# Kernel tuning notes

Hardware: AMD Instinct MI355X
Metric: run time of the kernel (lower is better)

## Reference

```python
import jax, jax.numpy as jnp
import numpy as np

N_HEAD = 16
D_MODEL = 1024
D_K = D_MODEL // N_HEAD  # 64
LN_EPS = 1e-5


def setup_inputs() -> dict:
    key = jax.random.key(0)
    ks = jax.random.split(key, 12)
    B, L, D = 4, 2048, D_MODEL
    std_qkv = float(np.sqrt(2.0 / (D + D_K)))
    q = jax.random.normal(ks[0], (B, L, D), jnp.float32)
    k = jax.random.normal(ks[1], (B, L, D), jnp.float32)
    v = jax.random.normal(ks[2], (B, L, D), jnp.float32)
    Wq = jax.random.normal(ks[3], (D, D), jnp.float32) * std_qkv
    Wk = jax.random.normal(ks[4], (D, D), jnp.float32) * std_qkv
    Wv = jax.random.normal(ks[5], (D, D), jnp.float32) * std_qkv
    bq = jnp.zeros((D,), jnp.float32)
    bk = jnp.zeros((D,), jnp.float32)
    bv = jnp.zeros((D,), jnp.float32)
    # xavier normal for fc: std = sqrt(2/(fan_in+fan_out))
    Wo = jax.random.normal(ks[6], (D, D), jnp.float32) * float(np.sqrt(2.0 / (D + D)))
    bo = jnp.zeros((D,), jnp.float32)
    gamma = jnp.ones((D,), jnp.float32)
    beta = jnp.zeros((D,), jnp.float32)
    return {"q": q, "k": k, "v": v, "Wq": Wq, "bq": bq, "Wk": Wk, "bk": bk,
            "Wv": Wv, "bv": bv, "Wo": Wo, "bo": bo, "gamma": gamma, "beta": beta}


def _layer_norm(x, gamma, beta):
    mu = jnp.mean(x, axis=-1, keepdims=True)
    var = jnp.mean(jnp.square(x - mu), axis=-1, keepdims=True)
    return (x - mu) * jax.lax.rsqrt(var + LN_EPS) * gamma + beta


def reference(q, k, v, Wq, bq, Wk, bk, Wv, bv, Wo, bo, gamma, beta):
    B, Lq, D = q.shape
    Lk = k.shape[1]
    h, dk = N_HEAD, D_K
    residual = q
    # projections (torch Linear: x @ W.T + b), split heads -> (h, b, l, dk)
    qh = (q @ Wq.T + bq).reshape(B, Lq, h, dk).transpose(2, 0, 1, 3)
    kh = (k @ Wk.T + bk).reshape(B, Lk, h, dk).transpose(2, 0, 1, 3)
    vh = (v @ Wv.T + bv).reshape(B, Lk, h, dk).transpose(2, 0, 1, 3)
    temp = jnp.asarray(np.power(dk, 0.5), qh.dtype)
    scores = jnp.einsum('hbqd,hbkd->hbqk', qh, kh) / temp
    attn = jax.nn.softmax(scores, axis=-1)  # softmax over key dim (dim=2 of bmm view)
    out = jnp.einsum('hbqk,hbkd->hbqd', attn, vh)
    # (h,b,lq,dk) -> (b,lq,h*dk)
    out = out.transpose(1, 2, 0, 3).reshape(B, Lq, D)
    out = out @ Wo.T + bo  # dropout p=0.0 -> identity
    out = _layer_norm(out + residual, gamma, beta)
    attn_flat = attn.reshape(h * B, Lq, Lk)  # matches torch (n_head*sz_b, lq, lk)
    return out, attn_flat
```

## Files before the change

### kernel.cpp

```cpp
#include <hip/hip_runtime.h>
#include <stdint.h>

typedef short bf16x8 __attribute__((ext_vector_type(8)));
typedef float f32x4 __attribute__((ext_vector_type(4)));
typedef unsigned short us4 __attribute__((ext_vector_type(4)));
typedef unsigned short us8 __attribute__((ext_vector_type(8)));
typedef unsigned uint2v __attribute__((ext_vector_type(2)));

#define SCL 0.18033688011112042f

__device__ __forceinline__ unsigned short f2bf(float f) {
  union { float f; unsigned u; } v; v.f = f;
  unsigned r = v.u + 0x7fffu + ((v.u >> 16) & 1u);
  return (unsigned short)(r >> 16);
}

__device__ __forceinline__ unsigned cvtpk(float lo, float hi) {
  unsigned r;
  asm("v_cvt_pk_bf16_f32 %0, %1, %2" : "=v"(r) : "v"(lo), "v"(hi));
  return r;
}

__device__ __forceinline__ float bf2f(unsigned short h) {
  union { unsigned u; float f; } v; v.u = ((unsigned)h) << 16; return v.f;
}

#define GL2LDS(g, l) __builtin_amdgcn_global_load_lds( \
    (const __attribute__((address_space(1))) void*)(g), \
    (__attribute__((address_space(3))) void*)(l), 16, 0, 0)

__global__ __launch_bounds__(256) void convert_all(
    const float* __restrict__ q, const float* __restrict__ k, const float* __restrict__ v,
    const float* __restrict__ wq, const float* __restrict__ wk, const float* __restrict__ wv,
    const float* __restrict__ wo,
    unsigned short* __restrict__ qb, unsigned short* __restrict__ kb, unsigned short* __restrict__ vb,
    unsigned short* __restrict__ wqb, unsigned short* __restrict__ wkb, unsigned short* __restrict__ wvb,
    unsigned short* __restrict__ wob)
{
  const long NB = 8388608, NW = 1048576;
  long i = ((long)blockIdx.x * 256 + threadIdx.x) * 4;
  if (i >= 3*NB + 4*NW) return;
  const float* src; unsigned short* dst; long off;
  if (i < NB)              { src = q;  dst = qb;  off = i; }
  else if (i < 2*NB)       { src = k;  dst = kb;  off = i - NB; }
  else if (i < 3*NB)       { src = v;  dst = vb;  off = i - 2*NB; }
  else if (i < 3*NB+NW)    { src = wq; dst = wqb; off = i - 3*NB; }
  else if (i < 3*NB+2*NW)  { src = wk; dst = wkb; off = i - 3*NB - NW; }
  else if (i < 3*NB+3*NW)  { src = wv; dst = wvb; off = i - 3*NB - 2*NW; }
  else                     { src = wo; dst = wob; off = i - 3*NB - 3*NW; }
  float4 x = *(const float4*)(src + off);
  us4 o; o.x = f2bf(x.x); o.y = f2bf(x.y); o.z = f2bf(x.z); o.w = f2bf(x.w);
  *(us4*)(dst + off) = o;
}

__global__ __launch_bounds__(256, 2) void qkv_gemm(
    const unsigned short* __restrict__ qb, const unsigned short* __restrict__ kb,
    const unsigned short* __restrict__ vb,
    const unsigned short* __restrict__ wqb, const unsigned short* __restrict__ wkb,
    const unsigned short* __restrict__ wvb,
    const float* __restrict__ bq, const float* __restrict__ bk, const float* __restrict__ bv,
    unsigned short* __restrict__ qh, unsigned short* __restrict__ kh,
    unsigned short* __restrict__ vt)
{
  const int z = blockIdx.z;
  const unsigned short* X = (z == 0) ? qb : (z == 1) ? kb : vb;
  const unsigned short* W = (z == 0) ? wqb : (z == 1) ? wkb : wvb;
  const float* bias = (z == 0) ? bq : (z == 1) ? bk : bv;
  unsigned short* dqh = (z == 0) ? qh : kh;
  const float sc = (z == 0) ? SCL : 1.0f;

  const int flat = blockIdx.x + (blockIdx.y << 6);
  const int xcd = flat & 7, ii = flat >> 3;
  const int m0 = (xcd * 8 + (ii & 7)) * 128;
  const int n0 = (ii >> 3) * 128;

  const int tid = threadIdx.x, lane = tid & 63, w = tid >> 6;
  const int wr = w >> 1, wc = w & 1;
  const int lg = lane >> 4, ll = lane & 15;

  __shared__ __align__(16) unsigned short As[2 * 128 * 32];
  __shared__ __align__(16) unsigned short Bs[2 * 128 * 32];

  f32x4 acc[4][4] = {};

  const char* gA = (const char*)X + ((size_t)(m0 + w*32 + (lane >> 2)) * 1024) * 2 + (lane & 3) * 16;
  const char* gB = (const char*)W + ((size_t)(n0 + w*32 + (lane >> 2)) * 1024) * 2 + (lane & 3) * 16;

#define STAGE_G(buf) do { \
    char* lA_ = (char*)As + (buf)*8192 + w*2048; \
    char* lB_ = (char*)Bs + (buf)*8192 + w*2048; \
    GL2LDS(gA, lA_); GL2LDS(gA + 32768, lA_ + 1024); \
    GL2LDS(gB, lB_); GL2LDS(gB + 32768, lB_ + 1024); \
    gA += 64; gB += 64; } while (0)

  STAGE_G(0);
  __syncthreads();

  for (int k0 = 0; k0 < 1024; k0 += 32) {
    const int cur = (k0 >> 5) & 1;
    if (k0 < 992) STAGE_G(cur ^ 1);
    const unsigned short* Ac = As + cur * 4096;
    const unsigned short* Bc = Bs + cur * 4096;
    bf16x8 xa[4], wb[4];
    const int kc = lg * 8;
#pragma unroll
    for (int f = 0; f < 4; ++f) xa[f] = *(const bf16x8*)&Ac[(wr*64 + f*16 + ll)*32 + kc];
#pragma unroll
    for (int f = 0; f < 4; ++f) wb[f] = *(const bf16x8*)&Bc[(wc*64 + f*16 + ll)*32 + kc];
    if (z < 2) {
#pragma unroll
      for (int fn = 0; fn < 4; ++fn)
#pragma unroll
        for (int fm = 0; fm < 4; ++fm)
          acc[fn][fm] = __builtin_amdgcn_mfma_f32_16x16x32_bf16(wb[fn], xa[fm], acc[fn][fm], 0, 0, 0);
    } else {
#pragma unroll
      for (int fm = 0; fm < 4; ++fm)
#pragma unroll
        for (int fn = 0; fn < 4; ++fn)
          acc[fm][fn] = __builtin_amdgcn_mfma_f32_16x16x32_bf16(xa[fm], wb[fn], acc[fm][fn], 0, 0, 0);
    }
    __syncthreads();
  }

  if (z < 2) {
#pragma unroll
    for (int fn = 0; fn < 4; ++fn) {
      const int n_g = n0 + wc*64 + fn*16 + lg*4;
      const float4 b4 = *(const float4*)&bias[n_g];
      const int h = n_g >> 6, dkk = n_g & 63;
#pragma unroll
      for (int fm = 0; fm < 4; ++fm) {
        const int m_g = m0 + wr*64 + fm*16 + ll;
        const int b_ = m_g >> 11, l_ = m_g & 2047;
        us4 pk;
        pk.x = f2bf((acc[fn][fm][0] + b4.x) * sc);
        pk.y = f2bf((acc[fn][fm][1] + b4.y) * sc);
        pk.z = f2bf((acc[fn][fm][2] + b4.z) * sc);
        pk.w = f2bf((acc[fn][fm][3] + b4.w) * sc);
        *(us4*)&dqh[((size_t)(h*4 + b_) * 2048 + l_) * 64 + dkk] = pk;
      }
    }
  } else {
#pragma unroll
    for (int fn = 0; fn < 4; ++fn) {
      const int n_g = n0 + wc*64 + fn*16 + ll;
      const float bias_n = bias[n_g];
      const int h = n_g >> 6, dkk = n_g & 63;
#pragma unroll
      for (int fm = 0; fm < 4; ++fm) {
        const int mrow = m0 + wr*64 + fm*16 + lg*4;
        const int b_ = mrow >> 11, l_ = mrow & 2047;
        us4 pk;
        pk.x = f2bf(acc[fm][fn][0] + bias_n);
        pk.y = f2bf(acc[fm][fn][1] + bias_n);
        pk.z = f2bf(acc[fm][fn][2] + bias_n);
        pk.w = f2bf(acc[fm][fn][3] + bias_n);
        *(us4*)&vt[((size_t)(h*4 + b_) * 64 + dkk) * 2048 + l_] = pk;
      }
    }
  }
}

__global__ __launch_bounds__(256, 2) void attn_kernel(
    const unsigned short* __restrict__ qh, const unsigned short* __restrict__ kh,
    const unsigned short* __restrict__ vt, float* __restrict__ probs,
    unsigned short* __restrict__ attn_o)
{
  const int bid = blockIdx.x;
  const int xcd = bid & 7;
  const int idx = bid >> 3;
  const int hb  = xcd * 8 + (idx & 7);
  const int qp  = idx >> 3;
  const int qt_a = qp * 2, qt_b = qp * 2 + 1;

  const int tid = threadIdx.x, lane = tid & 63, w = tid >> 6;
  const int wr = w >> 1, wc = w & 1;
  const int lg = lane >> 4, ll = lane & 15;

  __shared__ __align__(16) char smem[38400];
  unsigned short* Pb = (unsigned short*)smem;
  float* rs   = (float*)(smem + 36864);
  float* invl = (float*)(smem + 37888);
  float* Ored = (float*)smem;

  const size_t slab = (size_t)hb << 17;

  bf16x8 qfa[4][2], qfb[4][2];
#pragma unroll
  for (int fq = 0; fq < 4; ++fq)
#pragma unroll
    for (int dh = 0; dh < 2; ++dh) {
      qfa[fq][dh] = *(const bf16x8*)&qh[slab + (size_t)(qt_a*128 + wr*64 + fq*16 + ll)*64 + dh*32 + lg*8];
      qfb[fq][dh] = *(const bf16x8*)&qh[slab + (size_t)(qt_b*128 + wr*64 + fq*16 + ll)*64 + dh*32 + lg*8];
    }

  const unsigned short* Kf = kh + slab + (size_t)(wc*32 + ll)*64 + lg*8;
  const unsigned short* Vf = vt + slab + (size_t)ll*2048 + wc*32 + lg*8;

  const int prow = tid >> 4, pcol = (tid & 15) * 4;

  float rsum[4] = {0.f, 0.f, 0.f, 0.f};
  for (int kt = 0; kt < 32; ++kt) {
    bf16x8 ka[2][2];
#pragma unroll
    for (int fk = 0; fk < 2; ++fk)
#pragma unroll
      for (int dh = 0; dh < 2; ++dh)
        ka[fk][dh] = *(const bf16x8*)(Kf + kt*4096 + fk*1024 + dh*32);
    f32x4 s[2][4] = {};
    __builtin_amdgcn_s_setprio(1);
#pragma unroll
    for (int dh = 0; dh < 2; ++dh)
#pragma unroll
      for (int fk = 0; fk < 2; ++fk)
#pragma unroll
        for (int fq = 0; fq < 4; ++fq)
          s[fk][fq] = __builtin_amdgcn_mfma_f32_16x16x32_bf16(ka[fk][dh], qfa[fq][dh], s[fk][fq], 0, 0, 0);
    __builtin_amdgcn_s_setprio(0);
#pragma unroll
    for (int fk = 0; fk < 2; ++fk)
#pragma unroll
      for (int fq = 0; fq < 4; ++fq)
#pragma unroll
        for (int r = 0; r < 4; ++r)
          rsum[fq] += exp2f(s[fk][fq][r]);
  }

#pragma unroll
  for (int fq = 0; fq < 4; ++fq) {
    float t = rsum[fq];
    t += __shfl_xor(t, 16);
    t += __shfl_xor(t, 32);
    rsum[fq] = t;
  }
  if (lg == 0) {
#pragma unroll
    for (int fq = 0; fq < 4; ++fq)
      rs[wc*128 + wr*64 + fq*16 + ll] = rsum[fq];
  }
  __syncthreads();
  if (tid < 128) invl[tid] = 1.0f / (rs[tid] + rs[128 + tid]);
  __syncthreads();
  float inv_ra[4];
#pragma unroll
  for (int fq = 0; fq < 4; ++fq) inv_ra[fq] = invl[wr*64 + fq*16 + ll];
  __syncthreads();

  f32x4 o[4][4] = {};
  float rsb[4] = {0.f, 0.f, 0.f, 0.f};
  float* pb2a = probs + ((size_t)hb << 22) + (size_t)(qt_a*128) * 2048;

  for (int kt = 0; kt < 32; ++kt) {
    unsigned short* Pc = Pb + (kt & 1) * 9216;
    bf16x8 vb[4];
#pragma unroll
    for (int f = 0; f < 4; ++f)
      vb[f] = *(const bf16x8*)(Vf + f*32768 + kt*64);
    bf16x8 ka[2][2];
#pragma unroll
    for (int fk = 0; fk < 2; ++fk)
#pragma unroll
      for (int dh = 0; dh < 2; ++dh)
        ka[fk][dh] = *(const bf16x8*)(Kf + kt*4096 + fk*1024 + dh*32);

    {
      f32x4 sb[2][4] = {};
      __builtin_amdgcn_s_setprio(1);
#pragma unroll
      for (int dh = 0; dh < 2; ++dh)
#pragma unroll
        for (int fk = 0; fk < 2; ++fk)
#pragma unroll
          for (int fq = 0; fq < 4; ++fq)
            sb[fk][fq] = __builtin_amdgcn_mfma_f32_16x16x32_bf16(ka[fk][dh], qfb[fq][dh], sb[fk][fq], 0, 0, 0);
      __builtin_amdgcn_s_setprio(0);
#pragma unroll
      for (int fk = 0; fk < 2; ++fk)
#pragma unroll
        for (int fq = 0; fq < 4; ++fq)
#pragma unroll
          for (int r = 0; r < 4; ++r)
            rsb[fq] += exp2f(sb[fk][fq][r]);
    }

    f32x4 s[2][4] = {};
    __builtin_amdgcn_s_setprio(1);
#pragma unroll
    for (int dh = 0; dh < 2; ++dh)
#pragma unroll
      for (int fk = 0; fk < 2; ++fk)
#pragma unroll
        for (int fq = 0; fq < 4; ++fq)
          s[fk][fq] = __builtin_amdgcn_mfma_f32_16x16x32_bf16(ka[fk][dh], qfa[fq][dh], s[fk][fq], 0, 0, 0);
    __builtin_amdgcn_s_setprio(0);
#pragma unroll
    for (int fk = 0; fk < 2; ++fk)
#pragma unroll
      for (int fq = 0; fq < 4; ++fq) {
        float p0 = exp2f(s[fk][fq][0]) * inv_ra[fq];
        float p1 = exp2f(s[fk][fq][1]) * inv_ra[fq];
        float p2 = exp2f(s[fk][fq][2]) * inv_ra[fq];
        float p3 = exp2f(s[fk][fq][3]) * inv_ra[fq];
        uint2v u; u.x = cvtpk(p0, p1); u.y = cvtpk(p2, p3);
        *(uint2v*)&Pc[(wr*64 + fq*16 + ll)*72 + wc*32 + fk*16 + lg*4] = u;
      }
    __syncthreads();

    bf16x8 pa[4];
#pragma unroll
    for (int fm = 0; fm < 4; ++fm)
      pa[fm] = *(const bf16x8*)&Pc[(wr*64 + fm*16 + ll)*72 + wc*32 + lg*8];
    __builtin_amdgcn_s_setprio(1);
#pragma unroll
    for (int fm = 0; fm < 4; ++fm)
#pragma unroll
      for (int fd = 0; fd < 4; ++fd)
        o[fm][fd] = __builtin_amdgcn_mfma_f32_16x16x32_bf16(pa[fm], vb[fd], o[fm][fd], 0, 0, 0);
    __builtin_amdgcn_s_setprio(0);

    float* pdst = pb2a + kt*64;
#pragma unroll
    for (int j = 0; j < 8; ++j) {
      const int row = j*16 + prow;
      us4 pv = *(const us4*)&Pc[row*72 + pcol];
      f32x4 pf; pf[0] = bf2f(pv.x); pf[1] = bf2f(pv.y); pf[2] = bf2f(pv.z); pf[3] = bf2f(pv.w);
      __builtin_nontemporal_store(pf, (f32x4*)(pdst + (size_t)row*2048 + pcol));
    }
  }

  __syncthreads();
#pragma unroll
  for (int fq = 0; fq < 4; ++fq) {
    float t = rsb[fq];
    t += __shfl_xor(t, 16);
    t += __shfl_xor(t, 32);
    rsb[fq] = t;
  }
  if (lg == 0) {
#pragma unroll
    for (int fq = 0; fq < 4; ++fq)
      rs[wc*128 + wr*64 + fq*16 + ll] = rsb[fq];
  }
  if (wc == 1) {
#pragma unroll
    for (int fm = 0; fm < 4; ++fm)
#pragma unroll
      for (int fd = 0; fd < 4; ++fd)
#pragma unroll
        for (int r = 0; r < 4; ++r)
          Ored[wr*4096 + (fm*16 + lg*4 + r)*64 + fd*16 + ll] = o[fm][fd][r];
  }
  __syncthreads();
  if (tid < 128) invl[tid] = 1.0f / (rs[tid] + rs[128 + tid]);
  if (wc == 0) {
    const int b_ = hb & 3, h = hb >> 2;
#pragma unroll
    for (int fm = 0; fm < 4; ++fm)
#pragma unroll
      for (int fd = 0; fd < 4; ++fd)
#pragma unroll
        for (int r = 0; r < 4; ++r) {
          const int qrow = fm*16 + lg*4 + r;
          const int d = fd*16 + ll;
          float val = o[fm][fd][r] + Ored[wr*4096 + qrow*64 + d];
          const int mg = b_*2048 + qt_a*128 + wr*64 + qrow;
          attn_o[(size_t)mg*1024 + h*64 + d] = f2bf(val);
        }
  }
  __syncthreads();
  float inv_rb[4];
#pragma unroll
  for (int fq = 0; fq < 4; ++fq) inv_rb[fq] = invl[wr*64 + fq*16 + ll];
  __syncthreads();

#pragma unroll
  for (int fm = 0; fm < 4; ++fm)
#pragma unroll
    for (int fd = 0; fd < 4; ++fd)
      o[fm][fd] = f32x4{0.f, 0.f, 0.f, 0.f};
  float* pb2b = probs + ((size_t)hb << 22) + (size_t)(qt_b*128) * 2048;

  for (int kt = 0; kt < 32; ++kt) {
    unsigned short* Pc = Pb + (kt & 1) * 9216;
    bf16x8 vb[4];
#pragma unroll
    for (int f = 0; f < 4; ++f)
      vb[f] = *(const bf16x8*)(Vf + f*32768 + kt*64);
    bf16x8 ka[2][2];
#pragma unroll
    for (int fk = 0; fk < 2; ++fk)
#pragma unroll
      for (int dh = 0; dh < 2; ++dh)
        ka[fk][dh] = *(const bf16x8*)(Kf + kt*4096 + fk*1024 + dh*32);

    f32x4 s[2][4] = {};
    __builtin_amdgcn_s_setprio(1);
#pragma unroll
    for (int dh = 0; dh < 2; ++dh)
#pragma unroll
      for (int fk = 0; fk < 2; ++fk)
#pragma unroll
        for (int fq = 0; fq < 4; ++fq)
          s[fk][fq] = __builtin_amdgcn_mfma_f32_16x16x32_bf16(ka[fk][dh], qfb[fq][dh], s[fk][fq], 0, 0, 0);
    __builtin_amdgcn_s_setprio(0);

#pragma unroll
    for (int fk = 0; fk < 2; ++fk)
#pragma unroll
      for (int fq = 0; fq < 4; ++fq) {
        float p0 = exp2f(s[fk][fq][0]) * inv_rb[fq];
        float p1 = exp2f(s[fk][fq][1]) * inv_rb[fq];
        float p2 = exp2f(s[fk][fq][2]) * inv_rb[fq];
        float p3 = exp2f(s[fk][fq][3]) * inv_rb[fq];
        uint2v u; u.x = cvtpk(p0, p1); u.y = cvtpk(p2, p3);
        *(uint2v*)&Pc[(wr*64 + fq*16 + ll)*72 + wc*32 + fk*16 + lg*4] = u;
      }
    __syncthreads();

    bf16x8 pa[4];
#pragma unroll
    for (int fm = 0; fm < 4; ++fm)
      pa[fm] = *(const bf16x8*)&Pc[(wr*64 + fm*16 + ll)*72 + wc*32 + lg*8];
    __builtin_amdgcn_s_setprio(1);
#pragma unroll
    for (int fm = 0; fm < 4; ++fm)
#pragma unroll
      for (int fd = 0; fd < 4; ++fd)
        o[fm][fd] = __builtin_amdgcn_mfma_f32_16x16x32_bf16(pa[fm], vb[fd], o[fm][fd], 0, 0, 0);
    __builtin_amdgcn_s_setprio(0);

    float* pdst = pb2b + kt*64;
#pragma unroll
    for (int j = 0; j < 8; ++j) {
      const int row = j*16 + prow;
      us4 pv = *(const us4*)&Pc[row*72 + pcol];
      f32x4 pf; pf[0] = bf2f(pv.x); pf[1] = bf2f(pv.y); pf[2] = bf2f(pv.z); pf[3] = bf2f(pv.w);
      __builtin_nontemporal_store(pf, (f32x4*)(pdst + (size_t)row*2048 + pcol));
    }
  }

  __syncthreads();
  if (wc == 1) {
#pragma unroll
    for (int fm = 0; fm < 4; ++fm)
#pragma unroll
      for (int fd = 0; fd < 4; ++fd)
#pragma unroll
        for (int r = 0; r < 4; ++r)
          Ored[wr*4096 + (fm*16 + lg*4 + r)*64 + fd*16 + ll] = o[fm][fd][r];
  }
  __syncthreads();
  if (wc == 0) {
    const int b_ = hb & 3, h = hb >> 2;
#pragma unroll
    for (int fm = 0; fm < 4; ++fm)
#pragma unroll
      for (int fd = 0; fd < 4; ++fd)
#pragma unroll
        for (int r = 0; r < 4; ++r) {
          const int qrow = fm*16 + lg*4 + r;
          const int d = fd*16 + ll;
          float val = o[fm][fd][r] + Ored[wr*4096 + qrow*64 + d];
          const int mg = b_*2048 + qt_b*128 + wr*64 + qrow;
          attn_o[(size_t)mg*1024 + h*64 + d] = f2bf(val);
        }
  }
}

__global__ __launch_bounds__(256, 2) void outproj_gemm(
    const unsigned short* __restrict__ Ain, const unsigned short* __restrict__ Wob,
    const float* __restrict__ bo, const float* __restrict__ qres, float* __restrict__ preLN)
{
  const int flat = blockIdx.x + (blockIdx.y << 6);
  const int xcd = flat & 7, ii = flat >> 3;
  const int m0 = (xcd * 8 + (ii & 7)) * 128;
  const int n0 = (ii >> 3) * 128;

  const int tid = threadIdx.x, lane = tid & 63, w = tid >> 6;
  const int wr = w >> 1, wc = w & 1;
  const int lg = lane >> 4, ll = lane & 15;

  __shared__ __align__(16) unsigned short As[2 * 128 * 32];
  __shared__ __align__(16) unsigned short Bs[2 * 128 * 32];

  f32x4 acc[4][4] = {};

  const char* gA = (const char*)Ain + ((size_t)(m0 + w*32 + (lane >> 2)) * 1024) * 2 + (lane & 3) * 16;
  const char* gB = (const char*)Wob + ((size_t)(n0 + w*32 + (lane >> 2)) * 1024) * 2 + (lane & 3) * 16;

  STAGE_G(0);
  __syncthreads();

  for (int k0 = 0; k0 < 1024; k0 += 32) {
    const int cur = (k0 >> 5) & 1;
    if (k0 < 992) STAGE_G(cur ^ 1);
    const unsigned short* Ac = As + cur * 4096;
    const unsigned short* Bc = Bs + cur * 4096;
    bf16x8 xa[4], wb[4];
    const int kc = lg * 8;
#pragma unroll
    for (int f = 0; f < 4; ++f) xa[f] = *(const bf16x8*)&Ac[(wr*64 + f*16 + ll)*32 + kc];
#pragma unroll
    for (int f = 0; f < 4; ++f) wb[f] = *(const bf16x8*)&Bc[(wc*64 + f*16 + ll)*32 + kc];
#pragma unroll
    for (int fn = 0; fn < 4; ++fn)
#pragma unroll
      for (int fm = 0; fm < 4; ++fm)
        acc[fn][fm] = __builtin_amdgcn_mfma_f32_16x16x32_bf16(wb[fn], xa[fm], acc[fn][fm], 0, 0, 0);
    __syncthreads();
  }

#pragma unroll
  for (int fn = 0; fn < 4; ++fn) {
    const int n_g = n0 + wc*64 + fn*16 + lg*4;
    const float4 b4 = *(const float4*)&bo[n_g];
#pragma unroll
    for (int fm = 0; fm < 4; ++fm) {
      const int m_g = m0 + wr*64 + fm*16 + ll;
      const size_t idxp = (size_t)m_g * 1024 + n_g;
      const float4 r4 = *(const float4*)&qres[idxp];
      f32x4 y;
      y[0] = acc[fn][fm][0] + b4.x + r4.x;
      y[1] = acc[fn][fm][1] + b4.y + r4.y;
      y[2] = acc[fn][fm][2] + b4.z + r4.z;
      y[3] = acc[fn][fm][3] + b4.w + r4.w;
      *(f32x4*)&preLN[idxp] = y;
    }
  }
}

__global__ __launch_bounds__(256) void ln_kernel(
    const float* __restrict__ x, const float* __restrict__ gamma,
    const float* __restrict__ beta, float* __restrict__ out)
{
  const int row = blockIdx.x, tid = threadIdx.x;
  const float4 xv = ((const float4*)(x + (size_t)row * 1024))[tid];
  float s = xv.x + xv.y + xv.z + xv.w;
  float ss = xv.x*xv.x + xv.y*xv.y + xv.z*xv.z + xv.w*xv.w;
#pragma unroll
  for (int m = 1; m < 64; m <<= 1) { s += __shfl_xor(s, m); ss += __shfl_xor(ss, m); }
  __shared__ float red[8];
  if ((tid & 63) == 0) { red[(tid >> 6)*2] = s; red[(tid >> 6)*2 + 1] = ss; }
  __syncthreads();
  s  = red[0] + red[2] + red[4] + red[6];
  ss = red[1] + red[3] + red[5] + red[7];
  const float mu = s * (1.0f/1024.0f);
  const float var = ss * (1.0f/1024.0f) - mu*mu;
  const float rstd = rsqrtf(var + 1e-5f);
  const float4 g  = ((const float4*)gamma)[tid];
  const float4 be = ((const float4*)beta)[tid];
  float4 y;
  y.x = (xv.x - mu)*rstd*g.x + be.x;
  y.y = (xv.y - mu)*rstd*g.y + be.y;
  y.z = (xv.z - mu)*rstd*g.z + be.z;
  y.w = (xv.w - mu)*rstd*g.w + be.w;
  ((float4*)(out + (size_t)row * 1024))[tid] = y;
}

extern "C" void kernel_launch(void* const* d_in, const int* in_sizes, int n_in,
                              void* d_out, int out_size, void* d_ws, size_t ws_size,
                              hipStream_t stream) {
  const float* q     = (const float*)d_in[0];
  const float* k     = (const float*)d_in[1];
  const float* v     = (const float*)d_in[2];
  const float* Wq    = (const float*)d_in[3];
  const float* bq    = (const float*)d_in[4];
  const float* Wk    = (const float*)d_in[5];
  const float* bk    = (const float*)d_in[6];
  const float* Wv    = (const float*)d_in[7];
  const float* bv    = (const float*)d_in[8];
  const float* Wo    = (const float*)d_in[9];
  const float* bo    = (const float*)d_in[10];
  const float* gamma = (const float*)d_in[11];
  const float* beta  = (const float*)d_in[12];

  float* out   = (float*)d_out;
  float* probs = out + 8388608;

  char* ws = (char*)d_ws;
  unsigned short* qb  = (unsigned short*)(ws);
  unsigned short* kb  = (unsigned short*)(ws + 16777216);
  unsigned short* vb  = (unsigned short*)(ws + 33554432);
  unsigned short* wqb = (unsigned short*)(ws + 50331648);
  unsigned short* wkb = (unsigned short*)(ws + 52428800);
  unsigned short* wvb = (unsigned short*)(ws + 54525952);
  unsigned short* wob = (unsigned short*)(ws + 56623104);
  unsigned short* qh  = (unsigned short*)(ws + 58720256);
  unsigned short* kh  = (unsigned short*)(ws + 75497472);
  unsigned short* vt  = (unsigned short*)(ws + 92274688);
  float* preLN = (float*)(ws);
  unsigned short* attn_o = vb;

  convert_all<<<28672, 256, 0, stream>>>(q, k, v, Wq, Wk, Wv, Wo,
                                         qb, kb, vb, wqb, wkb, wvb, wob);

  dim3 g1(64, 8, 3);
  qkv_gemm<<<g1, 256, 0, stream>>>(qb, kb, vb, wqb, wkb, wvb, bq, bk, bv, qh, kh, vt);

  attn_kernel<<<512, 256, 0, stream>>>(qh, kh, vt, probs, attn_o);

  dim3 g3(64, 8);
  outproj_gemm<<<g3, 256, 0, stream>>>(attn_o, wob, bo, q, preLN);

  ln_kernel<<<8192, 256, 0, stream>>>(preLN, gamma, beta, out);
}
```

Baseline: 456.7 us.

## Stage GEMM epilogues through LDS for coalesced stores; reorder attention score passes

The QKV projection and output projection epilogues now write accumulator tiles into shared memory, reusing the operand buffers, and then re-read them so each thread stores 16-byte contiguous chunks to global memory. This replaces the scattered 8-byte strided stores for the head-split Q/K, the transposed V, and the fp32 pre-LayerNorm output with coalesced row writes. In the attention loop, the pass that writes normalized probabilities now runs before the row-sum pass for the next query tile, so the P tile is written to LDS earlier ahead of the barrier. The epilogues gain extra barriers and shared-memory traffic in exchange.

```diff
diff --git a/kernel.cpp b/kernel.cpp
--- a/kernel.cpp
+++ b/kernel.cpp
@@ -78,8 +78,10 @@
   const int wr = w >> 1, wc = w & 1;
   const int lg = lane >> 4, ll = lane & 15;
 
-  __shared__ __align__(16) unsigned short As[2 * 128 * 32];
-  __shared__ __align__(16) unsigned short Bs[2 * 128 * 32];
+  __shared__ __align__(16) char smem_q[32768];
+  unsigned short* As = (unsigned short*)smem_q;
+  unsigned short* Bs = (unsigned short*)(smem_q + 16384);
+  unsigned short* T  = (unsigned short*)smem_q;
 
   f32x4 acc[4][4] = {};
 
@@ -124,39 +126,69 @@
   }
 
   if (z < 2) {
-#pragma unroll
-    for (int fn = 0; fn < 4; ++fn) {
-      const int n_g = n0 + wc*64 + fn*16 + lg*4;
-      const float4 b4 = *(const float4*)&bias[n_g];
-      const int h = n_g >> 6, dkk = n_g & 63;
-#pragma unroll
-      for (int fm = 0; fm < 4; ++fm) {
-        const int m_g = m0 + wr*64 + fm*16 + ll;
-        const int b_ = m_g >> 11, l_ = m_g & 2047;
-        us4 pk;
-        pk.x = f2bf((acc[fn][fm][0] + b4.x) * sc);
-        pk.y = f2bf((acc[fn][fm][1] + b4.y) * sc);
-        pk.z = f2bf((acc[fn][fm][2] + b4.z) * sc);
-        pk.w = f2bf((acc[fn][fm][3] + b4.w) * sc);
-        *(us4*)&dqh[((size_t)(h*4 + b_) * 2048 + l_) * 64 + dkk] = pk;
+    const int b_ = m0 >> 11;
+#pragma unroll
+    for (int half = 0; half < 2; ++half) {
+      __syncthreads();
+      if (wr == half) {
+#pragma unroll
+        for (int fn = 0; fn < 4; ++fn) {
+          const int n_l = wc*64 + fn*16 + lg*4;
+          const float4 b4 = *(const float4*)&bias[n0 + n_l];
+#pragma unroll
+          for (int fm = 0; fm < 4; ++fm) {
+            us4 pk;
+            pk.x = f2bf((acc[fn][fm][0] + b4.x) * sc);
+            pk.y = f2bf((acc[fn][fm][1] + b4.y) * sc);
+            pk.z = f2bf((acc[fn][fm][2] + b4.z) * sc);
+            pk.w = f2bf((acc[fn][fm][3] + b4.w) * sc);
+            *(us4*)&T[(fm*16 + ll)*130 + n_l] = pk;
+          }
+        }
       }
+      __syncthreads();
+      const int seg = tid >> 3, off = (tid & 7) * 8;
+#pragma unroll
+      for (int it = 0; it < 4; ++it) {
+        const int s = it*32 + seg;
+        const int ml = s >> 1, nh = (s & 1) << 6;
+        us8 v = *(const us8*)&T[ml*130 + nh + off];
+        const int m_g = m0 + half*64 + ml;
+        const int l_ = m_g & 2047;
+        const int h = (n0 + nh) >> 6;
+        *(us8*)&dqh[((size_t)(h*4 + b_)*2048 + l_)*64 + off] = v;
+      }
     }
   } else {
-#pragma unroll
-    for (int fn = 0; fn < 4; ++fn) {
-      const int n_g = n0 + wc*64 + fn*16 + ll;
-      const float bias_n = bias[n_g];
-      const int h = n_g >> 6, dkk = n_g & 63;
-#pragma unroll
-      for (int fm = 0; fm < 4; ++fm) {
-        const int mrow = m0 + wr*64 + fm*16 + lg*4;
-        const int b_ = mrow >> 11, l_ = mrow & 2047;
-        us4 pk;
-        pk.x = f2bf(acc[fm][fn][0] + bias_n);
-        pk.y = f2bf(acc[fm][fn][1] + bias_n);
-        pk.z = f2bf(acc[fm][fn][2] + bias_n);
-        pk.w = f2bf(acc[fm][fn][3] + bias_n);
-        *(us4*)&vt[((size_t)(h*4 + b_) * 64 + dkk) * 2048 + l_] = pk;
+    const int b_ = m0 >> 11;
+#pragma unroll
+    for (int half = 0; half < 2; ++half) {
+      __syncthreads();
+      if (wc == half) {
+#pragma unroll
+        for (int fn = 0; fn < 4; ++fn) {
+          const float bias_n = bias[n0 + half*64 + fn*16 + ll];
+#pragma unroll
+          for (int fm = 0; fm < 4; ++fm) {
+            us4 pk;
+            pk.x = f2bf(acc[fm][fn][0] + bias_n);
+            pk.y = f2bf(acc[fm][fn][1] + bias_n);
+            pk.z = f2bf(acc[fm][fn][2] + bias_n);
+            pk.w = f2bf(acc[fm][fn][3] + bias_n);
+            *(us4*)&T[(fn*16 + ll)*130 + wr*64 + fm*16 + lg*4] = pk;
+          }
+        }
+      }
+      __syncthreads();
+      const int row = tid >> 4, mc = (tid & 15) * 8;
+#pragma unroll
+      for (int it = 0; it < 4; ++it) {
+        const int rr = it*16 + row;
+        us8 v = *(const us8*)&T[rr*130 + mc];
+        const int n_g = n0 + half*64 + rr;
+        const int h = n_g >> 6, dkk = n_g & 63;
+        const int l_ = (m0 + mc) & 2047;
+        *(us8*)&vt[((size_t)(h*4 + b_)*64 + dkk)*2048 + l_] = v;
       }
     }
   }
@@ -265,7 +297,7 @@
         ka[fk][dh] = *(const bf16x8*)(Kf + kt*4096 + fk*1024 + dh*32);
 
     {
-      f32x4 sb[2][4] = {};
+      f32x4 s[2][4] = {};
       __builtin_amdgcn_s_setprio(1);
 #pragma unroll
       for (int dh = 0; dh < 2; ++dh)
@@ -273,38 +305,40 @@
         for (int fk = 0; fk < 2; ++fk)
 #pragma unroll
           for (int fq = 0; fq < 4; ++fq)
-            sb[fk][fq] = __builtin_amdgcn_mfma_f32_16x16x32_bf16(ka[fk][dh], qfb[fq][dh], sb[fk][fq], 0, 0, 0);
+            s[fk][fq] = __builtin_amdgcn_mfma_f32_16x16x32_bf16(ka[fk][dh], qfa[fq][dh], s[fk][fq], 0, 0, 0);
       __builtin_amdgcn_s_setprio(0);
 #pragma unroll
       for (int fk = 0; fk < 2; ++fk)
 #pragma unroll
+        for (int fq = 0; fq < 4; ++fq) {
+          float p0 = exp2f(s[fk][fq][0]) * inv_ra[fq];
+          float p1 = exp2f(s[fk][fq][1]) * inv_ra[fq];
+          float p2 = exp2f(s[fk][fq][2]) * inv_ra[fq];
+          float p3 = exp2f(s[fk][fq][3]) * inv_ra[fq];
+          uint2v u; u.x = cvtpk(p0, p1); u.y = cvtpk(p2, p3);
+          *(uint2v*)&Pc[(wr*64 + fq*16 + ll)*72 + wc*32 + fk*16 + lg*4] = u;
+        }
+    }
+
+    {
+      f32x4 s[2][4] = {};
+      __builtin_amdgcn_s_setprio(1);
+#pragma unroll
+      for (int dh = 0; dh < 2; ++dh)
+#pragma unroll
+        for (int fk = 0; fk < 2; ++fk)
+#pragma unroll
+          for (int fq = 0; fq < 4; ++fq)
+            s[fk][fq] = __builtin_amdgcn_mfma_f32_16x16x32_bf16(ka[fk][dh], qfb[fq][dh], s[fk][fq], 0, 0, 0);
+      __builtin_amdgcn_s_setprio(0);
+#pragma unroll
+      for (int fk = 0; fk < 2; ++fk)
+#pragma unroll
         for (int fq = 0; fq < 4; ++fq)
 #pragma unroll
           for (int r = 0; r < 4; ++r)
-            rsb[fq] += exp2f(sb[fk][fq][r]);
-    }
-
-    f32x4 s[2][4] = {};
-    __builtin_amdgcn_s_setprio(1);
-#pragma unroll
-    for (int dh = 0; dh < 2; ++dh)
-#pragma unroll
-      for (int fk = 0; fk < 2; ++fk)
-#pragma unroll
-        for (int fq = 0; fq < 4; ++fq)
-          s[fk][fq] = __builtin_amdgcn_mfma_f32_16x16x32_bf16(ka[fk][dh], qfa[fq][dh], s[fk][fq], 0, 0, 0);
-    __builtin_amdgcn_s_setprio(0);
-#pragma unroll
-    for (int fk = 0; fk < 2; ++fk)
-#pragma unroll
-      for (int fq = 0; fq < 4; ++fq) {
-        float p0 = exp2f(s[fk][fq][0]) * inv_ra[fq];
-        float p1 = exp2f(s[fk][fq][1]) * inv_ra[fq];
-        float p2 = exp2f(s[fk][fq][2]) * inv_ra[fq];
-        float p3 = exp2f(s[fk][fq][3]) * inv_ra[fq];
-        uint2v u; u.x = cvtpk(p0, p1); u.y = cvtpk(p2, p3);
-        *(uint2v*)&Pc[(wr*64 + fq*16 + ll)*72 + wc*32 + fk*16 + lg*4] = u;
-      }
+            rsb[fq] += exp2f(s[fk][fq][r]);
+    }
     __syncthreads();
 
     bf16x8 pa[4];
@@ -481,8 +515,10 @@
   const int wr = w >> 1, wc = w & 1;
   const int lg = lane >> 4, ll = lane & 15;
 
-  __shared__ __align__(16) unsigned short As[2 * 128 * 32];
-  __shared__ __align__(16) unsigned short Bs[2 * 128 * 32];
+  __shared__ __align__(16) char smem_o[33792];
+  unsigned short* As = (unsigned short*)smem_o;
+  unsigned short* Bs = (unsigned short*)(smem_o + 16384);
+  float* Tf = (float*)smem_o;
 
   f32x4 acc[4][4] = {};
 
@@ -512,20 +548,34 @@
   }
 
 #pragma unroll
-  for (int fn = 0; fn < 4; ++fn) {
-    const int n_g = n0 + wc*64 + fn*16 + lg*4;
-    const float4 b4 = *(const float4*)&bo[n_g];
-#pragma unroll
-    for (int fm = 0; fm < 4; ++fm) {
-      const int m_g = m0 + wr*64 + fm*16 + ll;
-      const size_t idxp = (size_t)m_g * 1024 + n_g;
+  for (int half = 0; half < 2; ++half) {
+    __syncthreads();
+    if (wr == half) {
+#pragma unroll
+      for (int fn = 0; fn < 4; ++fn) {
+        const int n_l = wc*64 + fn*16 + lg*4;
+        const float4 b4 = *(const float4*)&bo[n0 + n_l];
+#pragma unroll
+        for (int fm = 0; fm < 4; ++fm) {
+          f32x4 y;
+          y[0] = acc[fn][fm][0] + b4.x;
+          y[1] = acc[fn][fm][1] + b4.y;
+          y[2] = acc[fn][fm][2] + b4.z;
+          y[3] = acc[fn][fm][3] + b4.w;
+          *(f32x4*)&Tf[(fm*16 + ll)*132 + n_l] = y;
+        }
+      }
+    }
+    __syncthreads();
+    const int r_ = tid >> 5, c_ = (tid & 31) * 4;
+#pragma unroll
+    for (int it = 0; it < 8; ++it) {
+      const int ml = it*8 + r_;
+      f32x4 v = *(const f32x4*)&Tf[ml*132 + c_];
+      const size_t idxp = (size_t)(m0 + half*64 + ml)*1024 + n0 + c_;
       const float4 r4 = *(const float4*)&qres[idxp];
-      f32x4 y;
-      y[0] = acc[fn][fm][0] + b4.x + r4.x;
-      y[1] = acc[fn][fm][1] + b4.y + r4.y;
-      y[2] = acc[fn][fm][2] + b4.z + r4.z;
-      y[3] = acc[fn][fm][3] + b4.w + r4.w;
-      *(f32x4*)&preLN[idxp] = y;
+      v[0] += r4.x; v[1] += r4.y; v[2] += r4.z; v[3] += r4.w;
+      *(f32x4*)&preLN[idxp] = v;
     }
   }
 }
```

New measurement: 448.2 us. Within noise of the previous version (-1.9%).
